# Kernel tuning notes

Hardware: AMD Instinct MI355X
Metric: run time of the kernel (lower is better)

## Reference

```python
import itertools
import jax, jax.numpy as jnp
import numpy as np

# static block configuration
B, C, H, W, DIM, HEADS = 2, 4, 60, 120, 512, 8
WS = (2, 6, 12)          # window size (Wc, Wh, Ww)
SS = (1, 3, 6)           # shift size
N = WS[0] * WS[1] * WS[2]            # 144 tokens per window
C1, H1, W1 = C // WS[0], H // WS[1], W // WS[2]
NW = C1 * H1 * W1                    # windows per sample
DH = DIM // HEADS
EPS = 1e-6


def _attn_bias():
    """Static shifted-window attention bias (nW, N, N): 0 within group, -inf across.
    Mirrors compute_3d_shifted_window_mask (warped=True, longitude wrap merge)."""
    img = np.zeros((C, H, W), np.int32)
    c_sl = ((0, C - WS[0]), (C - WS[0], C - SS[0]), (C - SS[0], C))
    h_sl = ((0, H - WS[1]), (H - WS[1], H - SS[1]), (H - SS[1], H))
    w_sl = ((0, W - WS[2]), (W - WS[2], W - SS[2]), (W - SS[2], W))
    cnt = 0
    for (cs, ce), (hs, he), (ws_, we) in itertools.product(c_sl, h_sl, w_sl):
        img[cs:ce, hs:he, ws_:we] = cnt
        cnt += 1
    # warped (periodic longitude) group merges
    for i in range(3):
        for a, b in ((1, 2), (4, 5), (7, 8)):
            img[img == a + 9 * i] = b + 9 * i
    m = img.reshape(C1, WS[0], H1, WS[1], W1, WS[2])
    m = m.transpose(0, 2, 4, 1, 3, 5).reshape(NW, N)
    diff = m[:, None, :] - m[:, :, None]
    return jnp.asarray(np.where(diff != 0, -np.inf, 0.0).astype(np.float32))


_BIAS = _attn_bias()[None, :, None, :, :]  # (1, nW, 1, N, N)


def _ln(x, s, b):
    mu = x.mean(-1, keepdims=True)
    var = x.var(-1, keepdims=True)
    return (x - mu) / jnp.sqrt(var + EPS) * s + b


def setup_inputs() -> dict:
    key = jax.random.key(0)
    ks = jax.random.split(key, 6)
    s = 0.02
    return {
        "x": jax.random.normal(ks[0], (B, C * H * W, DIM), jnp.float32),
        "qkv_w": jax.random.normal(ks[1], (DIM, 3 * DIM), jnp.float32) * s,
        "qkv_b": jnp.zeros((3 * DIM,), jnp.float32),
        "proj_w": jax.random.normal(ks[2], (DIM, DIM), jnp.float32) * s,
        "proj_b": jnp.zeros((DIM,), jnp.float32),
        "norm1_scale": jnp.ones((DIM,), jnp.float32),
        "norm1_bias": jnp.zeros((DIM,), jnp.float32),
        "norm2_scale": jnp.ones((DIM,), jnp.float32),
        "norm2_bias": jnp.zeros((DIM,), jnp.float32),
        "mlp_w1": jax.random.normal(ks[3], (DIM, 4 * DIM), jnp.float32) * s,
        "mlp_b1": jnp.zeros((4 * DIM,), jnp.float32),
        "mlp_w2": jax.random.normal(ks[4], (4 * DIM, DIM), jnp.float32) * s,
        "mlp_b2": jnp.zeros((DIM,), jnp.float32),
    }


def reference(x, qkv_w, qkv_b, proj_w, proj_b, norm1_scale, norm1_bias,
              norm2_scale, norm2_bias, mlp_w1, mlp_b1, mlp_w2, mlp_b2):
    shortcut = x                                   # (B, L, D)
    h = _ln(x, norm1_scale, norm1_bias).reshape(B, C, H, W, DIM)
    # cyclic shift
    h = jnp.roll(h, (-SS[0], -SS[1], -SS[2]), axis=(1, 2, 3))
    # window partition: (B,C,H,W,D) -> (B*nW, N, D)
    h = h.reshape(B, C1, WS[0], H1, WS[1], W1, WS[2], DIM)
    h = h.transpose(0, 1, 3, 5, 2, 4, 6, 7).reshape(B * NW, N, DIM)
    # windowed multi-head self-attention
    qkv = h @ qkv_w + qkv_b                        # (B*nW, N, 3*D)
    qkv = qkv.reshape(B, NW, N, 3, HEADS, DH)
    q = qkv[..., 0, :, :].transpose(0, 1, 3, 2, 4)  # (B, nW, H, N, Dh)
    k = qkv[..., 1, :, :].transpose(0, 1, 3, 2, 4)
    v = qkv[..., 2, :, :].transpose(0, 1, 3, 2, 4)
    scale = 1.0 / float(np.sqrt(DH))
    attn = jnp.einsum("bwhnd,bwhmd->bwhnm", q, k) * scale + _BIAS
    attn = jax.nn.softmax(attn, axis=-1)
    o = jnp.einsum("bwhnm,bwhmd->bwhnd", attn, v)
    o = o.transpose(0, 1, 3, 2, 4).reshape(B * NW, N, DIM)
    o = o @ proj_w + proj_b
    # window reverse: (B*nW, N, D) -> (B,C,H,W,D)
    o = o.reshape(B, C1, H1, W1, WS[0], WS[1], WS[2], DIM)
    o = o.transpose(0, 1, 4, 2, 5, 3, 6, 7).reshape(B, C, H, W, DIM)
    # reverse cyclic shift
    o = jnp.roll(o, SS, axis=(1, 2, 3))
    x = shortcut + o.reshape(B, C * H * W, DIM)    # drop_path is identity
    # MLP block
    h2 = _ln(x, norm2_scale, norm2_bias)
    h2 = jax.nn.gelu(h2 @ mlp_w1 + mlp_b1) @ mlp_w2 + mlp_b2
    return x + h2
```

## Files before the change

### kernel.cpp

```cpp
#include <hip/hip_runtime.h>

typedef __attribute__((ext_vector_type(8))) short bf16x8;
typedef __attribute__((ext_vector_type(4))) float f32x4;
typedef __attribute__((ext_vector_type(8))) unsigned short u16x8;

#define BARX() asm volatile("s_barrier" ::: "memory")
#define VMC(n) asm volatile("s_waitcnt vmcnt(" #n ")" ::: "memory")

__device__ inline unsigned short f2bf(float f) {
  unsigned int u = __float_as_uint(f);
  u += 0x7fffu + ((u >> 16) & 1u);
  return (unsigned short)(u >> 16);
}

__device__ inline void gload_lds16(const void* g, void* l) {
  __builtin_amdgcn_global_load_lds(
      (const __attribute__((address_space(1))) void*)g,
      (__attribute__((address_space(3))) void*)l, 16, 0, 0);
}

__global__ void wtrans(const float* __restrict__ W, unsigned short* __restrict__ Wt,
                       int K, int N) {
  int idx = blockIdx.x * 256 + threadIdx.x;
  if (idx >= K * N) return;
  int k = idx / N, n = idx - k * N;
  Wt[(size_t)n * K + k] = f2bf(W[idx]);
}

template <int MODE>
__global__ void ln_k(const float* __restrict__ x, const float* __restrict__ sc,
                     const float* __restrict__ bi, unsigned short* __restrict__ o) {
  int t = blockIdx.x * 4 + (threadIdx.x >> 6);
  int l = threadIdx.x & 63;
  size_t src;
  if (MODE == 0) {
    int b = t / 28800, r = t - b * 28800;
    int win = r / 144, tok = r - win * 144;
    int c1 = win / 100, rem = win - c1 * 100;
    int h1 = rem / 10, w1 = rem - h1 * 10;
    int tc = tok / 72, tr = tok - tc * 72;
    int th = tr / 12, tw = tr - th * 12;
    int cs = c1 * 2 + tc, hs = h1 * 6 + th, wsp = w1 * 12 + tw;
    int co = (cs + 1) & 3;
    int ho = hs + 3; if (ho >= 60) ho -= 60;
    int wo = wsp + 6; if (wo >= 120) wo -= 120;
    src = ((size_t)b * 28800 + (co * 60 + ho) * 120 + wo) * 512;
  } else {
    src = (size_t)t * 512;
  }
  const float4* xr = (const float4*)(x + src);
  float4 v0 = xr[l * 2], v1 = xr[l * 2 + 1];
  float s = v0.x + v0.y + v0.z + v0.w + v1.x + v1.y + v1.z + v1.w;
  float s2 = v0.x * v0.x + v0.y * v0.y + v0.z * v0.z + v0.w * v0.w +
             v1.x * v1.x + v1.y * v1.y + v1.z * v1.z + v1.w * v1.w;
  #pragma unroll
  for (int o2 = 32; o2; o2 >>= 1) {
    s += __shfl_xor(s, o2);
    s2 += __shfl_xor(s2, o2);
  }
  float mean = s * (1.0f / 512.0f);
  float var = s2 * (1.0f / 512.0f) - mean * mean;
  float inv = rsqrtf(var + 1e-6f);
  const float4* scp = (const float4*)sc;
  const float4* bip = (const float4*)bi;
  float4 sa = scp[l * 2], sb = scp[l * 2 + 1];
  float4 ba = bip[l * 2], bb = bip[l * 2 + 1];
  u16x8 ov;
  ov[0] = f2bf((v0.x - mean) * inv * sa.x + ba.x);
  ov[1] = f2bf((v0.y - mean) * inv * sa.y + ba.y);
  ov[2] = f2bf((v0.z - mean) * inv * sa.z + ba.z);
  ov[3] = f2bf((v0.w - mean) * inv * sa.w + ba.w);
  ov[4] = f2bf((v1.x - mean) * inv * sb.x + bb.x);
  ov[5] = f2bf((v1.y - mean) * inv * sb.y + bb.y);
  ov[6] = f2bf((v1.z - mean) * inv * sb.z + bb.z);
  ov[7] = f2bf((v1.w - mean) * inv * sb.w + bb.w);
  *(u16x8*)&o[(size_t)t * 512 + l * 8] = ov;
}

template <int EPI>
__launch_bounds__(512, 2)
__global__ void gemm256(const unsigned short* __restrict__ A,
                        const unsigned short* __restrict__ Bt,
                        const float* __restrict__ bias, void* __restrict__ outp,
                        const float* __restrict__ res, int M, int N, int K) {
  __shared__ __attribute__((aligned(16))) unsigned short lds[4][2][8192];
  const int tid = threadIdx.x;
  const int w = tid >> 6, l = tid & 63;
  const int wm = w >> 2, wn = w & 3;
  const int lane15 = l & 15, lk = (l >> 4) << 3;
  const int ntile = N >> 8;
  const int bm = blockIdx.x / ntile, bn = blockIdx.x - bm * ntile;
  const int KT = K >> 6;
  const unsigned short* Ag = A + (size_t)bm * 256 * K;
  const unsigned short* Bg = Bt + (size_t)bn * 256 * K;
  const int lq = l >> 2;
  const int sc0 = (l & 3) << 3;

  f32x4 acc[8][4] = {};

  auto STAGE = [&](int c, int part) {
    const unsigned short* gb = part ? Bg : Ag;
    unsigned short* lb = (unsigned short*)&lds[c & 3][part][0];
    const int kc = c << 5;
    #pragma unroll
    for (int i = 0; i < 2; ++i) {
      int j = i * 8 + w;
      int row = j * 16 + lq;
      int sc = sc0 ^ (((row >> 1) & 3) << 3);
      gload_lds16(gb + (size_t)row * K + kc + sc, lb + j * 512);
    }
  };
  auto LDA4 = [&](bf16x8* af, int c, int mq) {
    const unsigned short* p = &lds[c & 3][0][0];
    #pragma unroll
    for (int mf = 0; mf < 4; ++mf) {
      int row = wm * 128 + (mq * 4 + mf) * 16 + lane15;
      af[mf] = *(const bf16x8*)&p[row * 32 + (lk ^ (((row >> 1) & 3) << 3))];
    }
  };
  auto LDB4 = [&](bf16x8* bfr, int c) {
    const unsigned short* p = &lds[c & 3][1][0];
    #pragma unroll
    for (int nf = 0; nf < 4; ++nf) {
      int row = wn * 64 + nf * 16 + lane15;
      bfr[nf] = *(const bf16x8*)&p[row * 32 + (lk ^ (((row >> 1) & 3) << 3))];
    }
  };
  auto MFMA16 = [&](bf16x8* af, bf16x8* bfr, int mq) {
    __builtin_amdgcn_s_setprio(1);
    #pragma unroll
    for (int mf = 0; mf < 4; ++mf)
      #pragma unroll
      for (int nf = 0; nf < 4; ++nf)
        acc[mq * 4 + mf][nf] = __builtin_amdgcn_mfma_f32_16x16x32_bf16(
            af[mf], bfr[nf], acc[mq * 4 + mf][nf], 0, 0, 0);
    __builtin_amdgcn_s_setprio(0);
  };

  STAGE(0, 0); STAGE(0, 1); STAGE(1, 0); STAGE(1, 1); STAGE(2, 0); STAGE(2, 1);
  VMC(8);
  BARX();

  for (int t = 0; t < KT; ++t) {
    const int c0 = 2 * t, c1 = c0 + 1;
    const bool s01 = (t <= KT - 2), s23 = (t <= KT - 3);
    bf16x8 af[4], bfr[4];
    LDA4(af, c0, 0); LDB4(bfr, c0);
    if (s01) STAGE(c0 + 3, 0);
    BARX();
    MFMA16(af, bfr, 0);
    BARX();
    LDA4(af, c0, 1);
    if (s01) STAGE(c0 + 3, 1);
    BARX();
    MFMA16(af, bfr, 1);
    if (t <= KT - 2) { VMC(8); } else { VMC(0); }
    BARX();
    LDA4(af, c1, 0); LDB4(bfr, c1);
    if (s23) STAGE(c0 + 4, 0);
    BARX();
    MFMA16(af, bfr, 0);
    BARX();
    LDA4(af, c1, 1);
    if (s23) STAGE(c0 + 4, 1);
    BARX();
    MFMA16(af, bfr, 1);
    if (s23) { VMC(8); } else if (t == KT - 2) { VMC(4); }
    BARX();
  }

  float* outf = (float*)outp;
  unsigned short* outh = (unsigned short*)outp;
  #pragma unroll
  for (int mi = 0; mi < 8; ++mi) {
    #pragma unroll
    for (int j = 0; j < 4; ++j) {
      int grow = bm * 256 + wm * 128 + mi * 16 + ((l >> 4) << 2) + j;
      int win = 0, tok = 0;
      size_t rowbase = 0;
      if constexpr (EPI == 0) {
        win = grow / 144;
        tok = grow - win * 144;
      } else if constexpr (EPI == 1) {
        win = grow / 144;
        tok = grow - win * 144;
        int b = win / 200, wl = win - b * 200;
        int c1 = wl / 100, rem = wl - c1 * 100;
        int h1 = rem / 10, w1 = rem - h1 * 10;
        int tc = tok / 72, tr = tok - tc * 72;
        int th = tr / 12, tw = tr - th * 12;
        int cs = c1 * 2 + tc, hs = h1 * 6 + th, wsp = w1 * 12 + tw;
        int co = (cs + 1) & 3;
        int ho = hs + 3; if (ho >= 60) ho -= 60;
        int wo = wsp + 6; if (wo >= 120) wo -= 120;
        rowbase = ((size_t)b * 28800 + (co * 60 + ho) * 120 + wo) * 512;
      }
      #pragma unroll
      for (int nf = 0; nf < 4; ++nf) {
        int gcol = bn * 256 + wn * 64 + nf * 16 + lane15;
        float val = acc[mi][nf][j] + bias[gcol];
        if constexpr (EPI == 0) {
          int which = gcol >> 9, hd = (gcol >> 6) & 7, dh = gcol & 63;
          outh[(((size_t)(win * 3 + which) * 8 + hd) * 144 + tok) * 64 + dh] = f2bf(val);
        } else if constexpr (EPI == 1) {
          size_t oi = rowbase + gcol;
          outf[oi] = res[oi] + val;
        } else if constexpr (EPI == 2) {
          float u = 0.7978845608f * (val + 0.044715f * val * val * val);
          float g = val / (1.0f + __expf(-2.0f * u));
          outh[(size_t)grow * N + gcol] = f2bf(g);
        } else {
          size_t oi = (size_t)grow * N + gcol;
          outf[oi] += val;
        }
      }
    }
  }
}

__launch_bounds__(576)
__global__ void attn_k(const unsigned short* __restrict__ qkv,
                       unsigned short* __restrict__ owin) {
  __shared__ __attribute__((aligned(16))) unsigned short Ks[144 * 72];
  __shared__ __attribute__((aligned(16))) unsigned short Vt[64 * 168];
  __shared__ __attribute__((aligned(16))) unsigned short Ps[144 * 168];
  __shared__ unsigned char gid[144];
  int bid = blockIdx.x;
  int win = bid >> 3, head = bid & 7;
  const unsigned short* qb = qkv + ((size_t)(win * 3 + 0) * 8 + head) * (144 * 64);
  const unsigned short* kb = qkv + ((size_t)(win * 3 + 1) * 8 + head) * (144 * 64);
  const unsigned short* vb = qkv + ((size_t)(win * 3 + 2) * 8 + head) * (144 * 64);
  int tid = threadIdx.x;
  {
    int row = tid >> 2, c0 = (tid & 3) << 4;
    u16x8 ka = *(const u16x8*)(kb + row * 64 + c0);
    u16x8 kc = *(const u16x8*)(kb + row * 64 + c0 + 8);
    *(u16x8*)&Ks[row * 72 + c0] = ka;
    *(u16x8*)&Ks[row * 72 + c0 + 8] = kc;
    u16x8 va = *(const u16x8*)(vb + row * 64 + c0);
    u16x8 vc = *(const u16x8*)(vb + row * 64 + c0 + 8);
    #pragma unroll
    for (int j = 0; j < 8; ++j) Vt[(c0 + j) * 168 + row] = va[j];
    #pragma unroll
    for (int j = 0; j < 8; ++j) Vt[(c0 + 8 + j) * 168 + row] = vc[j];
  }
  for (int i = tid; i < 64 * 24; i += 576) {
    int d = i / 24, m = i - d * 24;
    Vt[d * 168 + 144 + m] = 0;
  }
  for (int i = tid; i < 144 * 24; i += 576) {
    int r = i / 24, c = i - r * 24;
    Ps[r * 168 + 144 + c] = 0;
  }
  if (tid < 144) {
    int wl = win % 200;
    int c1 = wl / 100, rem = wl - c1 * 100;
    int h1 = rem / 10, w1 = rem - h1 * 10;
    int tc = tid / 72, tr = tid - tc * 72;
    int th = tr / 12, tw = tr - th * 12;
    int cs = c1 * 2 + tc, hs = h1 * 6 + th, wsp = w1 * 12 + tw;
    int rc = cs < 2 ? 0 : (cs < 3 ? 1 : 2);
    int rh = hs < 54 ? 0 : (hs < 57 ? 1 : 2);
    int rw = wsp < 108 ? 0 : (wsp < 114 ? 1 : 2);
    if (rw == 1) rw = 2;
    gid[tid] = (unsigned char)(rc * 9 + rh * 3 + rw);
  }
  __syncthreads();
  int wv = tid >> 6, l = tid & 63;
  int lane15 = l & 15, lk = (l >> 4) << 3;
  bf16x8 aq0 = *(const bf16x8*)(qb + (wv * 16 + lane15) * 64 + lk);
  bf16x8 aq1 = *(const bf16x8*)(qb + (wv * 16 + lane15) * 64 + 32 + lk);
  f32x4 sf[9];
  #pragma unroll
  for (int ct = 0; ct < 9; ++ct) {
    f32x4 z = {};
    bf16x8 b0 = *(const bf16x8*)&Ks[(ct * 16 + lane15) * 72 + lk];
    bf16x8 b1 = *(const bf16x8*)&Ks[(ct * 16 + lane15) * 72 + 32 + lk];
    z = __builtin_amdgcn_mfma_f32_16x16x32_bf16(aq0, b0, z, 0, 0, 0);
    z = __builtin_amdgcn_mfma_f32_16x16x32_bf16(aq1, b1, z, 0, 0, 0);
    sf[ct] = z;
  }
  int gi[4];
  #pragma unroll
  for (int j = 0; j < 4; ++j) gi[j] = gid[wv * 16 + ((l >> 4) << 2) + j];
  float mx[4] = {-1e30f, -1e30f, -1e30f, -1e30f};
  #pragma unroll
  for (int ct = 0; ct < 9; ++ct) {
    int gj = gid[ct * 16 + lane15];
    #pragma unroll
    for (int j = 0; j < 4; ++j) {
      float s = sf[ct][j] * 0.125f;
      if (gj != gi[j]) s = -1e30f;
      sf[ct][j] = s;
      mx[j] = fmaxf(mx[j], s);
    }
  }
  #pragma unroll
  for (int o2 = 8; o2; o2 >>= 1)
    #pragma unroll
    for (int j = 0; j < 4; ++j) mx[j] = fmaxf(mx[j], __shfl_xor(mx[j], o2));
  float sm[4] = {0.f, 0.f, 0.f, 0.f};
  #pragma unroll
  for (int ct = 0; ct < 9; ++ct)
    #pragma unroll
    for (int j = 0; j < 4; ++j) {
      float e = __expf(sf[ct][j] - mx[j]);
      sf[ct][j] = e;
      sm[j] += e;
    }
  #pragma unroll
  for (int o2 = 8; o2; o2 >>= 1)
    #pragma unroll
    for (int j = 0; j < 4; ++j) sm[j] += __shfl_xor(sm[j], o2);
  float rs[4];
  #pragma unroll
  for (int j = 0; j < 4; ++j) rs[j] = 1.0f / sm[j];
  #pragma unroll
  for (int ct = 0; ct < 9; ++ct)
    #pragma unroll
    for (int j = 0; j < 4; ++j)
      Ps[(wv * 16 + ((l >> 4) << 2) + j) * 168 + ct * 16 + lane15] =
          f2bf(sf[ct][j] * rs[j]);
  __syncthreads();
  f32x4 of[4] = {};
  #pragma unroll
  for (int ks = 0; ks < 5; ++ks) {
    bf16x8 ap = *(const bf16x8*)&Ps[(wv * 16 + lane15) * 168 + ks * 32 + lk];
    #pragma unroll
    for (int nt = 0; nt < 4; ++nt) {
      bf16x8 bv = *(const bf16x8*)&Vt[(nt * 16 + lane15) * 168 + ks * 32 + lk];
      of[nt] = __builtin_amdgcn_mfma_f32_16x16x32_bf16(ap, bv, of[nt], 0, 0, 0);
    }
  }
  unsigned short* ob = owin + (size_t)win * 144 * 512 + head * 64;
  #pragma unroll
  for (int nt = 0; nt < 4; ++nt)
    #pragma unroll
    for (int j = 0; j < 4; ++j) {
      int row = wv * 16 + ((l >> 4) << 2) + j;
      ob[(size_t)row * 512 + nt * 16 + lane15] = f2bf(of[nt][j]);
    }
}

extern "C" void kernel_launch(void* const* d_in, const int* in_sizes, int n_in,
                              void* d_out, int out_size, void* d_ws, size_t ws_size,
                              hipStream_t stream) {
  const float* x = (const float*)d_in[0];
  const float* qkv_w = (const float*)d_in[1];
  const float* qkv_b = (const float*)d_in[2];
  const float* proj_w = (const float*)d_in[3];
  const float* proj_b = (const float*)d_in[4];
  const float* n1s = (const float*)d_in[5];
  const float* n1b = (const float*)d_in[6];
  const float* n2s = (const float*)d_in[7];
  const float* n2b = (const float*)d_in[8];
  const float* w1 = (const float*)d_in[9];
  const float* b1 = (const float*)d_in[10];
  const float* w2 = (const float*)d_in[11];
  const float* b2 = (const float*)d_in[12];
  float* out = (float*)d_out;
  char* ws = (char*)d_ws;

  unsigned short* WqT = (unsigned short*)(ws);
  unsigned short* WpT = (unsigned short*)(ws + 1572864);
  unsigned short* W1T = (unsigned short*)(ws + 2097152);
  unsigned short* W2T = (unsigned short*)(ws + 4194304);
  unsigned short* hwin = (unsigned short*)(ws + 6291456);
  unsigned short* qkvb = (unsigned short*)(ws + 65273856);
  unsigned short* owin = (unsigned short*)(ws + 242221056);
  unsigned short* mid = qkvb;

  wtrans<<<(512 * 1536 + 255) / 256, 256, 0, stream>>>(qkv_w, WqT, 512, 1536);
  wtrans<<<(512 * 512 + 255) / 256, 256, 0, stream>>>(proj_w, WpT, 512, 512);
  wtrans<<<(512 * 2048 + 255) / 256, 256, 0, stream>>>(w1, W1T, 512, 2048);
  wtrans<<<(2048 * 512 + 255) / 256, 256, 0, stream>>>(w2, W2T, 2048, 512);
  ln_k<0><<<14400, 256, 0, stream>>>(x, n1s, n1b, hwin);
  gemm256<0><<<225 * 6, 512, 0, stream>>>(hwin, WqT, qkv_b, qkvb, nullptr, 57600, 1536, 512);
  attn_k<<<3200, 576, 0, stream>>>(qkvb, owin);
  gemm256<1><<<225 * 2, 512, 0, stream>>>(owin, WpT, proj_b, out, x, 57600, 512, 512);
  ln_k<1><<<14400, 256, 0, stream>>>(out, n2s, n2b, hwin);
  gemm256<2><<<225 * 8, 512, 0, stream>>>(hwin, W1T, b1, mid, nullptr, 57600, 2048, 512);
  gemm256<3><<<225 * 2, 512, 0, stream>>>(mid, W2T, b2, out, nullptr, 57600, 512, 2048);
}
```

Baseline: 933.3 us.

## Unroll GEMM main loop with static LDS slots, inline ds_reads and XCD-aware block remap

Rewrites the gemm256 mainloop so it is unrolled four chunks per iteration with compile-time LDS slot offsets. Fragment loads become inline-asm ds_read_b128 with immediate offsets from precomputed base addresses, and explicit lgkmcnt waits plus sched_barriers order them against the MFMAs. It also remaps block IDs so consecutive tiles land on the same XCD, which should improve L2 reuse. The aim is to cut address arithmetic and modulo slot indexing and to raise cache locality. In exchange it hard-codes the pipeline tail, assumes K is a multiple of 128 with at least 2 iterations, and the asm constraints could limit compiler scheduling.

```diff
diff --git a/kernel.cpp b/kernel.cpp
--- a/kernel.cpp
+++ b/kernel.cpp
@@ -4,8 +4,10 @@
 typedef __attribute__((ext_vector_type(4))) float f32x4;
 typedef __attribute__((ext_vector_type(8))) unsigned short u16x8;
 
-#define BARX() asm volatile("s_barrier" ::: "memory")
+#define BAR() __builtin_amdgcn_s_barrier()
 #define VMC(n) asm volatile("s_waitcnt vmcnt(" #n ")" ::: "memory")
+#define WAITL() do { asm volatile("s_waitcnt lgkmcnt(0)"); __builtin_amdgcn_sched_barrier(0); } while (0)
+#define DSR(dst, a, off) asm volatile("ds_read_b128 %0, %1 offset:" #off : "=&v"(dst) : "v"(a))
 
 __device__ inline unsigned short f2bf(float f) {
   unsigned int u = __float_as_uint(f);
@@ -86,87 +88,118 @@
   __shared__ __attribute__((aligned(16))) unsigned short lds[4][2][8192];
   const int tid = threadIdx.x;
   const int w = tid >> 6, l = tid & 63;
-  const int wm = w >> 2, wn = w & 3;
+  const int wm = (tid >> 8) & 1, wn = (tid >> 6) & 3;
   const int lane15 = l & 15, lk = (l >> 4) << 3;
   const int ntile = N >> 8;
-  const int bm = blockIdx.x / ntile, bn = blockIdx.x - bm * ntile;
-  const int KT = K >> 6;
+  const int nwg = gridDim.x;
+  const int q = nwg >> 3, r = nwg & 7;
+  const int xcd = blockIdx.x & 7, idx8 = blockIdx.x >> 3;
+  const int wgid = (xcd < r ? xcd * (q + 1) : r * (q + 1) + (xcd - r) * q) + idx8;
+  const int bm = wgid / ntile, bn = wgid - bm * ntile;
   const unsigned short* Ag = A + (size_t)bm * 256 * K;
   const unsigned short* Bg = Bt + (size_t)bn * 256 * K;
   const int lq = l >> 2;
   const int sc0 = (l & 3) << 3;
+  const int scs = sc0 ^ (((lq >> 1) & 3) << 3);
+  const int sw = ((lane15 >> 1) & 3) << 3;
+
+  unsigned lds0 = (unsigned)(unsigned long long)
+      (__attribute__((address_space(3))) void*)(void*)&lds[0][0][0];
+  const unsigned aA = lds0 + (unsigned)((wm * 128 + lane15) * 64 + ((lk ^ sw) << 1));
+  const unsigned aB = lds0 + 16384u + (unsigned)((wn * 64 + lane15) * 64 + ((lk ^ sw) << 1));
 
   f32x4 acc[8][4] = {};
-
-  auto STAGE = [&](int c, int part) {
+  bf16x8 af[4], bfr[4];
+
+  auto STAGE = [&](int slot, int part, int c) {
     const unsigned short* gb = part ? Bg : Ag;
-    unsigned short* lb = (unsigned short*)&lds[c & 3][part][0];
+    unsigned short* lb = &lds[0][0][0] + slot * 16384 + part * 8192;
     const int kc = c << 5;
     #pragma unroll
     for (int i = 0; i < 2; ++i) {
       int j = i * 8 + w;
       int row = j * 16 + lq;
-      int sc = sc0 ^ (((row >> 1) & 3) << 3);
-      gload_lds16(gb + (size_t)row * K + kc + sc, lb + j * 512);
+      gload_lds16(gb + (size_t)row * K + kc + scs, lb + j * 512);
     }
   };
-  auto LDA4 = [&](bf16x8* af, int c, int mq) {
-    const unsigned short* p = &lds[c & 3][0][0];
-    #pragma unroll
-    for (int mf = 0; mf < 4; ++mf) {
-      int row = wm * 128 + (mq * 4 + mf) * 16 + lane15;
-      af[mf] = *(const bf16x8*)&p[row * 32 + (lk ^ (((row >> 1) & 3) << 3))];
-    }
+  auto LDA4 = [&](unsigned base) {
+    DSR(af[0], base, 0);
+    DSR(af[1], base, 1024);
+    DSR(af[2], base, 2048);
+    DSR(af[3], base, 3072);
   };
-  auto LDB4 = [&](bf16x8* bfr, int c) {
-    const unsigned short* p = &lds[c & 3][1][0];
-    #pragma unroll
-    for (int nf = 0; nf < 4; ++nf) {
-      int row = wn * 64 + nf * 16 + lane15;
-      bfr[nf] = *(const bf16x8*)&p[row * 32 + (lk ^ (((row >> 1) & 3) << 3))];
-    }
+  auto LDB4 = [&](unsigned base) {
+    DSR(bfr[0], base, 0);
+    DSR(bfr[1], base, 1024);
+    DSR(bfr[2], base, 2048);
+    DSR(bfr[3], base, 3072);
   };
-  auto MFMA16 = [&](bf16x8* af, bf16x8* bfr, int mq) {
+  auto MFMA16 = [&](int h) {
     __builtin_amdgcn_s_setprio(1);
     #pragma unroll
     for (int mf = 0; mf < 4; ++mf)
       #pragma unroll
       for (int nf = 0; nf < 4; ++nf)
-        acc[mq * 4 + mf][nf] = __builtin_amdgcn_mfma_f32_16x16x32_bf16(
-            af[mf], bfr[nf], acc[mq * 4 + mf][nf], 0, 0, 0);
+        acc[h * 4 + mf][nf] = __builtin_amdgcn_mfma_f32_16x16x32_bf16(
+            af[mf], bfr[nf], acc[h * 4 + mf][nf], 0, 0, 0);
     __builtin_amdgcn_s_setprio(0);
   };
 
-  STAGE(0, 0); STAGE(0, 1); STAGE(1, 0); STAGE(1, 1); STAGE(2, 0); STAGE(2, 1);
+  const int NI = K >> 7;
+
+  STAGE(0, 0, 0); STAGE(0, 1, 0);
+  STAGE(1, 0, 1); STAGE(1, 1, 1);
+  STAGE(2, 0, 2); STAGE(2, 1, 2);
   VMC(8);
-  BARX();
-
-  for (int t = 0; t < KT; ++t) {
-    const int c0 = 2 * t, c1 = c0 + 1;
-    const bool s01 = (t <= KT - 2), s23 = (t <= KT - 3);
-    bf16x8 af[4], bfr[4];
-    LDA4(af, c0, 0); LDB4(bfr, c0);
-    if (s01) STAGE(c0 + 3, 0);
-    BARX();
-    MFMA16(af, bfr, 0);
-    BARX();
-    LDA4(af, c0, 1);
-    if (s01) STAGE(c0 + 3, 1);
-    BARX();
-    MFMA16(af, bfr, 1);
-    if (t <= KT - 2) { VMC(8); } else { VMC(0); }
-    BARX();
-    LDA4(af, c1, 0); LDB4(bfr, c1);
-    if (s23) STAGE(c0 + 4, 0);
-    BARX();
-    MFMA16(af, bfr, 0);
-    BARX();
-    LDA4(af, c1, 1);
-    if (s23) STAGE(c0 + 4, 1);
-    BARX();
-    MFMA16(af, bfr, 1);
-    if (s23) { VMC(8); } else if (t == KT - 2) { VMC(4); }
-    BARX();
+  BAR();
+
+  for (int i = 0; i < NI - 1; ++i) {
+    const int c4 = 4 * i;
+    LDA4(aA + 0 * 32768 + 0); LDB4(aB + 0 * 32768);
+    STAGE(3, 0, c4 + 3);
+    BAR(); WAITL(); MFMA16(0); BAR();
+    LDA4(aA + 0 * 32768 + 4096);
+    STAGE(3, 1, c4 + 3);
+    BAR(); WAITL(); MFMA16(1); VMC(8); BAR();
+    LDA4(aA + 1 * 32768 + 0); LDB4(aB + 1 * 32768);
+    STAGE(0, 0, c4 + 4);
+    BAR(); WAITL(); MFMA16(0); BAR();
+    LDA4(aA + 1 * 32768 + 4096);
+    STAGE(0, 1, c4 + 4);
+    BAR(); WAITL(); MFMA16(1); VMC(8); BAR();
+    LDA4(aA + 2 * 32768 + 0); LDB4(aB + 2 * 32768);
+    STAGE(1, 0, c4 + 5);
+    BAR(); WAITL(); MFMA16(0); BAR();
+    LDA4(aA + 2 * 32768 + 4096);
+    STAGE(1, 1, c4 + 5);
+    BAR(); WAITL(); MFMA16(1); VMC(8); BAR();
+    LDA4(aA + 3 * 32768 + 0); LDB4(aB + 3 * 32768);
+    STAGE(2, 0, c4 + 6);
+    BAR(); WAITL(); MFMA16(0); BAR();
+    LDA4(aA + 3 * 32768 + 4096);
+    STAGE(2, 1, c4 + 6);
+    BAR(); WAITL(); MFMA16(1); VMC(8); BAR();
+  }
+  {
+    const int c4 = 4 * (NI - 1);
+    LDA4(aA + 0 * 32768 + 0); LDB4(aB + 0 * 32768);
+    STAGE(3, 0, c4 + 3);
+    BAR(); WAITL(); MFMA16(0); BAR();
+    LDA4(aA + 0 * 32768 + 4096);
+    STAGE(3, 1, c4 + 3);
+    BAR(); WAITL(); MFMA16(1); VMC(8); BAR();
+    LDA4(aA + 1 * 32768 + 0); LDB4(aB + 1 * 32768);
+    BAR(); WAITL(); MFMA16(0); BAR();
+    LDA4(aA + 1 * 32768 + 4096);
+    BAR(); WAITL(); MFMA16(1); VMC(4); BAR();
+    LDA4(aA + 2 * 32768 + 0); LDB4(aB + 2 * 32768);
+    BAR(); WAITL(); MFMA16(0); BAR();
+    LDA4(aA + 2 * 32768 + 4096);
+    BAR(); WAITL(); MFMA16(1); VMC(0); BAR();
+    LDA4(aA + 3 * 32768 + 0); LDB4(aB + 3 * 32768);
+    BAR(); WAITL(); MFMA16(0); BAR();
+    LDA4(aA + 3 * 32768 + 4096);
+    BAR(); WAITL(); MFMA16(1); BAR();
   }
 
   float* outf = (float*)outp;
```

Measured after the change: 881.5 us. 5.5% less time.
